# Performance work log

Hardware: AMD Instinct MI355X
Metric: run time of the kernel (lower is better)

## Reference

```python
import jax, jax.numpy as jnp
import numpy as np

INF = 1000000.0
B, S, D = 4, 1024, 768
NH, DH = 12, 64
LN_EPS = 1e-9


def _relative_shift_gather(pos_attn, context_len, shift):
    # pos_attn: [b, n, seq_len, max_rel_len]
    b, n, s, m = pos_attn.shape
    x = pos_attn.reshape(b, n, m, s)[:, :, shift:, :]
    x = x.reshape(b, n, s, m - shift)[..., :context_len]
    return x


def setup_inputs() -> dict:
    key = jax.random.key(0)
    ks = jax.random.split(key, 24)
    std = 0.02
    inp = {
        'query': jax.random.normal(ks[0], (B, S, D), jnp.float32),
        'key': jax.random.normal(ks[1], (B, S, D), jnp.float32),
        'value': jax.random.normal(ks[2], (B, S, D), jnp.float32),
        'r': jax.random.normal(ks[3], (2 * S - 1, D), jnp.float32),
        'token_type_mat': jax.random.randint(ks[4], (B, S, S), 0, 2) > 0,
        'attention_mask': jnp.ones((B, S), jnp.int32),
        'cls_mask': jnp.ones((1, 1, S, S), jnp.float32),
        'Wq': jax.random.normal(ks[5], (D, NH * DH), jnp.float32) * std,
        'Wk': jax.random.normal(ks[6], (D, NH * DH), jnp.float32) * std,
        'bk': jnp.zeros((NH * DH,), jnp.float32),
        'Wv': jax.random.normal(ks[7], (D, NH * DH), jnp.float32) * std,
        'bv': jnp.zeros((NH * DH,), jnp.float32),
        'Wpost': jax.random.normal(ks[8], (NH * DH, D), jnp.float32) * std,
        'bpost': jnp.zeros((D,), jnp.float32),
        'ln_g': jnp.ones((D,), jnp.float32),
        'ln_b': jnp.zeros((D,), jnp.float32),
        'r_w_bias': jax.random.normal(ks[9], (NH, DH), jnp.float32) * std,
        'r_r_bias': jax.random.normal(ks[10], (NH, DH), jnp.float32) * std,
        'r_kernel': jax.random.normal(ks[11], (D, NH, DH), jnp.float32) * std,
        'r_s_bias': jax.random.normal(ks[12], (NH, DH), jnp.float32) * std,
        'seg_embed': jax.random.normal(ks[13], (2, NH, DH), jnp.float32) * std,
    }
    return inp


def reference(query, key, value, r, token_type_mat, attention_mask, cls_mask,
              Wq, Wk, bk, Wv, bv, Wpost, bpost, ln_g, ln_b,
              r_w_bias, r_r_bias, r_kernel, r_s_bias, seg_embed):
    b, s, d_model = query.shape
    n_head, d_head = r_w_bias.shape
    context_len = key.shape[1]
    scale = 1.0 / d_head ** 0.5

    q_head = (query @ Wq).reshape(b, s, n_head, d_head) * scale   # bind
    k_head = (key @ Wk + bk).reshape(b, context_len, n_head, d_head)
    v_head = (value @ Wv + bv).reshape(b, context_len, n_head, d_head)

    # content score
    content_score = jnp.einsum('bind,bjnd->bnij', q_head + r_w_bias * scale, k_head)

    # relative positional attention (relative_shift path, shift=1 since s == context_len)
    shift = 2 if s != context_len else 1
    r_head = jnp.einsum('td,dnh->tnh', r, r_kernel)
    positional_attn = jnp.einsum('binh,tnh->bnit', q_head + r_r_bias * scale, r_head)
    positional_attn = _relative_shift_gather(positional_attn, context_len, shift)
    positional_attn = positional_attn * cls_mask

    # relative token-type (segment) attention
    token_type_bias = jnp.einsum('bind,snd->bnis', q_head + r_s_bias * scale, seg_embed)
    diff_tt = token_type_bias[..., 0:1]  # [b,n,i,1]
    same_tt = token_type_bias[..., 1:2]
    token_type_attn = jnp.where(token_type_mat[:, None], same_tt, diff_tt) * cls_mask

    attn_score = content_score + positional_attn + token_type_attn
    attn_score = attn_score - INF * (1.0 - attention_mask[:, None, None].astype(jnp.float32))
    attn_prob = jax.nn.softmax(attn_score, axis=-1)

    attn_vec = jnp.einsum('bnij,bjnd->bind', attn_prob, v_head)
    attn_out = attn_vec.reshape(b, s, n_head * d_head) @ Wpost + bpost

    x = query + attn_out
    mean = jnp.mean(x, axis=-1, keepdims=True)
    var = jnp.var(x, axis=-1, keepdims=True)
    out = (x - mean) * jax.lax.rsqrt(var + LN_EPS) * ln_g + ln_b
    return out
```

## Files before the change

kernel.cpp:

```cpp
#include <hip/hip_runtime.h>
#include <hip/hip_bf16.h>

#define S_LEN   1024
#define D_MODEL 768
#define N_HEAD  12
#define D_HEAD  64
#define BATCH   4
#define T_LEN   2047
#define INF_VAL 1000000.0f
#define SCALE   0.125f
#define LN_EPSF 1e-9f

typedef __attribute__((ext_vector_type(8))) __bf16 bf8;
typedef __attribute__((ext_vector_type(4))) __bf16 bf4;
typedef __attribute__((ext_vector_type(4))) float  f32x4;

__device__ __forceinline__ int swz_addr(int row, int byte_in_row) {
    return ((row << 7) + byte_in_row) ^ ((row & 7) << 4);
}

#define GLOAD_LDS(gsrc, ldst) \
    __builtin_amdgcn_global_load_lds( \
        (const __attribute__((address_space(1))) void*)(gsrc), \
        (__attribute__((address_space(3))) void*)(ldst), 16, 0, 0)

__global__ void detect_kernel(const unsigned char* __restrict__ p, int* __restrict__ flag)
{
    int lane = threadIdx.x;
    int nz = 0;
    int base = lane * 64;
    for (int k = base; k < base + 64; k += 4)
        nz += (p[k+1] != 0) + (p[k+2] != 0) + (p[k+3] != 0);
    unsigned long long m = __ballot(nz != 0);
    if (lane == 0) { flag[0] = (m == 0ull) ? 1 : 0; flag[1] = 1; }
}

__global__ __launch_bounds__(256)
void tobf16_kernel(const float* __restrict__ q, const float* __restrict__ k,
                   const float* __restrict__ v, const float* __restrict__ r,
                   __bf16* __restrict__ qb, __bf16* __restrict__ kb,
                   __bf16* __restrict__ vb, __bf16* __restrict__ rb)
{
    int z = blockIdx.z;
    const float* src; __bf16* dst; size_t n;
    if (z == 0)      { src = q; dst = qb; n = (size_t)4096*768; }
    else if (z == 1) { src = k; dst = kb; n = (size_t)4096*768; }
    else if (z == 2) { src = v; dst = vb; n = (size_t)4096*768; }
    else             { src = r; dst = rb; n = (size_t)T_LEN*768; }
    size_t i = ((size_t)blockIdx.x * 256 + threadIdx.x) * 8;
    if (i + 8 > n) return;
    float4 a = *(const float4*)(src + i);
    float4 b = *(const float4*)(src + i + 4);
    bf8 o;
    o[0]=(__bf16)a.x; o[1]=(__bf16)a.y; o[2]=(__bf16)a.z; o[3]=(__bf16)a.w;
    o[4]=(__bf16)b.x; o[5]=(__bf16)b.y; o[6]=(__bf16)b.z; o[7]=(__bf16)b.w;
    *(bf8*)(dst + i) = o;
}

__global__ __launch_bounds__(256)
void prep_sel(const void* __restrict__ ttm, const int* __restrict__ flag,
              unsigned char* __restrict__ selbit)
{
    size_t idx = ((size_t)blockIdx.x * 256 + threadIdx.x) * 8;
    unsigned long long out = 0;
    if (flag[0]) {
        const int* ip = (const int*)ttm + idx;
        int4 a = *(const int4*)ip;
        int4 b = *(const int4*)(ip + 4);
        out  = (a.x ? 1ull : 0)       | (a.y ? 1ull : 0) << 8
             | (a.z ? 1ull : 0) << 16 | (a.w ? 1ull : 0) << 24
             | (b.x ? 1ull : 0) << 32 | (b.y ? 1ull : 0) << 40
             | (b.z ? 1ull : 0) << 48 | (b.w ? 1ull : 0) << 56;
    } else {
        unsigned long long raw = *(const unsigned long long*)((const unsigned char*)ttm + idx);
        #pragma unroll
        for (int i = 0; i < 8; ++i)
            out |= (((raw >> (8*i)) & 0xffull) ? 1ull : 0) << (8*i);
    }
    *(unsigned long long*)(selbit + idx) = out;
}

__global__ __launch_bounds__(256)
void clsb_prep(const float* __restrict__ cls, const int* __restrict__ amask,
               __bf16* __restrict__ clsb, float* __restrict__ maskadd,
               int* __restrict__ flag)
{
    size_t idx = ((size_t)blockIdx.x * 256 + threadIdx.x) * 8;
    const float* p = cls + idx;
    float4 a = *(const float4*)p;
    float4 b = *(const float4*)(p + 4);
    bf8 o;
    o[0]=(__bf16)a.x; o[1]=(__bf16)a.y; o[2]=(__bf16)a.z; o[3]=(__bf16)a.w;
    o[4]=(__bf16)b.x; o[5]=(__bf16)b.y; o[6]=(__bf16)b.z; o[7]=(__bf16)b.w;
    *(bf8*)(clsb + idx) = o;
    int ok = (a.x==1.f)&&(a.y==1.f)&&(a.z==1.f)&&(a.w==1.f)
          && (b.x==1.f)&&(b.y==1.f)&&(b.z==1.f)&&(b.w==1.f);
    if (blockIdx.x == 0) {
        for (int j = threadIdx.x; j < BATCH * S_LEN; j += 256) {
            int am = amask[j];
            maskadd[j] = -INF_VAL * (1.f - (float)am);
            ok &= (am == 1);
        }
    }
    ok = __syncthreads_and(ok);
    if (threadIdx.x == 0 && !ok) atomicAnd(flag + 1, 0);
}

__global__ __launch_bounds__(256)
void wtrans_kernel(const float* __restrict__ W0, const float* __restrict__ W1,
                   const float* __restrict__ W2, const float* __restrict__ W3,
                   const float* __restrict__ W4,
                   __bf16* __restrict__ T0, __bf16* __restrict__ T1,
                   __bf16* __restrict__ T2, __bf16* __restrict__ T3,
                   __bf16* __restrict__ T4)
{
    const float* W; __bf16* Wt;
    switch (blockIdx.z) {
        case 0: W = W0; Wt = T0; break;
        case 1: W = W1; Wt = T1; break;
        case 2: W = W2; Wt = T2; break;
        case 3: W = W3; Wt = T3; break;
        default: W = W4; Wt = T4; break;
    }
    const int K = 768, N = 768;
    __shared__ float tile[64][65];
    int tid = threadIdx.x;
    int r = tid >> 4, c4 = (tid & 15) * 4;
    int k0 = blockIdx.y * 64, n0 = blockIdx.x * 64;
    #pragma unroll
    for (int rep = 0; rep < 4; ++rep) {
        int row = rep * 16 + r;
        float4 v = *(const float4*)(W + (size_t)(k0 + row) * N + n0 + c4);
        tile[row][c4+0] = v.x; tile[row][c4+1] = v.y;
        tile[row][c4+2] = v.z; tile[row][c4+3] = v.w;
    }
    __syncthreads();
    #pragma unroll
    for (int rep = 0; rep < 4; ++rep) {
        int row = rep * 16 + r;
        bf4 o;
        #pragma unroll
        for (int j = 0; j < 4; ++j) o[j] = (__bf16)tile[c4 + j][row];
        *(bf4*)(Wt + (size_t)(n0 + row) * K + k0 + c4) = o;
    }
}

__device__ __forceinline__
void gemm_tile_body(const __bf16* __restrict__ A, const __bf16* __restrict__ Bt,
                    const float* __restrict__ bias, void* __restrict__ C,
                    int M, int N, int K, float scale, int has_bias,
                    int out_mode, int m0, int n0, __bf16* As, __bf16* Bs)
{
    int tid = threadIdx.x;
    int lane = tid & 63, w = tid >> 6;
    int grp = lane >> 4, lcol = lane & 15;
    int wm = w >> 1, wn = w & 1;

    auto loadA = [&](int kt, int rep) -> bf8 {
        int id = rep * 256 + tid;
        int row = id >> 3, ch = id & 7;
        int gm = m0 + row; if (gm >= M) gm = M - 1;
        return *(const bf8*)(A + (size_t)gm * K + kt + ch * 8);
    };
    auto loadB = [&](int kt, int rep) -> bf8 {
        int id = rep * 256 + tid;
        int row = id >> 3, ch = id & 7;
        return *(const bf8*)(Bt + (size_t)(n0 + row) * K + kt + ch * 8);
    };

    bf8 aR0 = loadA(0,0), aR1 = loadA(0,1), aR2 = loadA(0,2), aR3 = loadA(0,3);
    bf8 bR0 = loadB(0,0), bR1 = loadB(0,1), bR2 = loadB(0,2), bR3 = loadB(0,3);

    f32x4 acc[4][4] = {};

    for (int kt = 0; kt < K; kt += 64) {
        __syncthreads();
        {
            int id0 = tid;
            { int id = 0*256 + id0; int row = id >> 3, ch = id & 7;
              *(bf8*)((char*)As + swz_addr(row, ch*16)) = aR0;
              *(bf8*)((char*)Bs + swz_addr(row, ch*16)) = bR0; }
            { int id = 1*256 + id0; int row = id >> 3, ch = id & 7;
              *(bf8*)((char*)As + swz_addr(row, ch*16)) = aR1;
              *(bf8*)((char*)Bs + swz_addr(row, ch*16)) = bR1; }
            { int id = 2*256 + id0; int row = id >> 3, ch = id & 7;
              *(bf8*)((char*)As + swz_addr(row, ch*16)) = aR2;
              *(bf8*)((char*)Bs + swz_addr(row, ch*16)) = bR2; }
            { int id = 3*256 + id0; int row = id >> 3, ch = id & 7;
              *(bf8*)((char*)As + swz_addr(row, ch*16)) = aR3;
              *(bf8*)((char*)Bs + swz_addr(row, ch*16)) = bR3; }
        }
        __syncthreads();
        if (kt + 64 < K) {
            aR0 = loadA(kt+64,0); aR1 = loadA(kt+64,1); aR2 = loadA(kt+64,2); aR3 = loadA(kt+64,3);
            bR0 = loadB(kt+64,0); bR1 = loadB(kt+64,1); bR2 = loadB(kt+64,2); bR3 = loadB(kt+64,3);
        }
        #pragma unroll
        for (int kk = 0; kk < 2; ++kk) {
            bf8 a[4], bb[4];
            #pragma unroll
            for (int mi = 0; mi < 4; ++mi)
                a[mi] = *(const bf8*)((const char*)As + swz_addr(wm * 64 + mi * 16 + lcol, kk * 64 + grp * 16));
            #pragma unroll
            for (int ni = 0; ni < 4; ++ni)
                bb[ni] = *(const bf8*)((const char*)Bs + swz_addr(wn * 64 + ni * 16 + lcol, kk * 64 + grp * 16));
            #pragma unroll
            for (int mi = 0; mi < 4; ++mi) {
                #pragma unroll
                for (int ni = 0; ni < 4; ++ni)
                    acc[mi][ni] = __builtin_amdgcn_mfma_f32_16x16x32_bf16(a[mi], bb[ni], acc[mi][ni], 0, 0, 0);
            }
        }
    }

    #pragma unroll
    for (int ni = 0; ni < 4; ++ni) {
        int col = n0 + wn * 64 + ni * 16 + lcol;
        float bval = has_bias ? bias[col] : 0.f;
        #pragma unroll
        for (int mi = 0; mi < 4; ++mi) {
            int rbase = m0 + wm * 64 + mi * 16 + grp * 4;
            if (out_mode == 2) {
                int hn = col >> 6, d = col & 63;
                int bb2 = rbase >> 10;
                int j = rbase & 1023;
                bf4 o;
                #pragma unroll
                for (int reg = 0; reg < 4; ++reg)
                    o[reg] = (__bf16)(acc[mi][ni][reg] * scale + bval);
                *(bf4*)((__bf16*)C + ((size_t)(bb2 * N_HEAD + hn) * 64 + d) * 1024 + j) = o;
            } else {
                #pragma unroll
                for (int reg = 0; reg < 4; ++reg) {
                    int row = rbase + reg;
                    if (row < M) {
                        float vv = acc[mi][ni][reg] * scale + bval;
                        if (out_mode == 1) ((__bf16*)C)[(size_t)row * N + col] = (__bf16)vv;
                        else               ((float*)C)[(size_t)row * N + col] = vv;
                    }
                }
            }
        }
    }
}

__global__ __launch_bounds__(256, 3)
void proj_gemm(const __bf16* __restrict__ qb, const __bf16* __restrict__ kb,
               const __bf16* __restrict__ vb, const __bf16* __restrict__ rb,
               const __bf16* __restrict__ Wqt, const __bf16* __restrict__ Wkt,
               const __bf16* __restrict__ Wvt, const __bf16* __restrict__ rkt,
               const float* __restrict__ bk, const float* __restrict__ bv,
               __bf16* __restrict__ qh, __bf16* __restrict__ kh,
               __bf16* __restrict__ vhT, __bf16* __restrict__ rhd)
{
    __shared__ __align__(16) __bf16 As[128 * 64];
    __shared__ __align__(16) __bf16 Bs[128 * 64];
    int id = blockIdx.x;
    int wg = (id & 7) * 96 + (id >> 3);
    int z  = wg / 192;
    int rem = wg % 192;
    int by = rem / 6, bx = rem % 6;

    const __bf16* A; const __bf16* Bt; const float* bias; void* C;
    int M; float scale; int has_bias; int omode;
    if (z == 0)      { A = qb; Bt = Wqt; bias = nullptr; C = qh;  M = 4096; scale = SCALE; has_bias = 0; omode = 1; }
    else if (z == 1) { A = kb; Bt = Wkt; bias = bk;      C = kh;  M = 4096; scale = 1.f;   has_bias = 1; omode = 1; }
    else if (z == 2) { A = vb; Bt = Wvt; bias = bv;      C = vhT; M = 4096; scale = 1.f;   has_bias = 1; omode = 2; }
    else             { A = rb; Bt = rkt; bias = nullptr; C = rhd; M = T_LEN; scale = 1.f;  has_bias = 0; omode = 1; }
    int m0 = by * 128, n0 = bx * 128;
    if (m0 >= M) return;
    gemm_tile_body(A, Bt, bias, C, M, 768, 768, scale, has_bias, omode, m0, n0, As, Bs);
}

__global__ __launch_bounds__(256, 3)
void post_gemm(const __bf16* __restrict__ av, const __bf16* __restrict__ Wpt,
               const float* __restrict__ bpost, float* __restrict__ ao)
{
    __shared__ __align__(16) __bf16 As[128 * 64];
    __shared__ __align__(16) __bf16 Bs[128 * 64];
    int id = blockIdx.x;
    int wg = (id & 7) * 24 + (id >> 3);
    int by = wg / 6, bx = wg % 6;
    gemm_tile_body(av, Wpt, bpost, ao, 4096, 768, 768, 1.f, 1, 0,
                   by * 128, bx * 128, As, Bs);
}

__global__ __launch_bounds__(256)
void ttbias_kernel(const __bf16* __restrict__ qh, const float* __restrict__ rsb,
                   const float* __restrict__ seg, float* __restrict__ tt)
{
    int idx = blockIdx.x * 256 + threadIdx.x;
    if (idx >= BATCH * S_LEN * N_HEAD * 2) return;
    int s2  = idx & 1;
    int n   = (idx >> 1) % N_HEAD;
    int row = idx / (2 * N_HEAD);
    const __bf16* q  = qh  + (size_t)row * D_MODEL + n * D_HEAD;
    const float* sg = seg + ((size_t)s2 * N_HEAD + n) * D_HEAD;
    const float* rb = rsb + n * D_HEAD;
    float s = 0.f;
    for (int h = 0; h < D_HEAD; ++h) s += ((float)q[h] + rb[h] * SCALE) * sg[h];
    tt[idx] = s;
}

__global__ __launch_bounds__(256, 3)
void attn_kernel(const __bf16* __restrict__ qh, const __bf16* __restrict__ kh,
                 const __bf16* __restrict__ vhT, const __bf16* __restrict__ rhd,
                 const float* __restrict__ tt, const __bf16* __restrict__ clsb,
                 const unsigned char* __restrict__ selbit,
                 const float* __restrict__ maskadd,
                 const float* __restrict__ rwb, const float* __restrict__ rrb,
                 const int* __restrict__ flag, __bf16* __restrict__ av)
{
    __shared__ __align__(16) __bf16 Kt[64*64];
    __shared__ __align__(16) __bf16 Vt[64*64];
    __shared__ __align__(16) __bf16 Rw[128*64];
    __shared__ __align__(16) __bf16 Ps[4*16*64];
    __shared__ __align__(16) __bf16 poss[4*16*84];

    int tid = threadIdx.x;
    int i0 = blockIdx.x * 64;
    int n  = blockIdx.y;
    int b  = blockIdx.z;
    int bS = b * S_LEN;
    int n64 = n * D_HEAD;
    int simple = flag[1];

    int lane = tid & 63, w = tid >> 6;
    int grp = lane >> 4, lcol = lane & 15;

    const __bf16* vT = vhT + (size_t)(b * N_HEAD + n) * 64 * 1024;

    int srow = tid >> 3;
    int koff = (((tid & 7) * 16) ^ ((srow & 7) << 4)) >> 1;

    bf8 qwA[2], qrA[2];
    {
        size_t qrow = (size_t)(bS + i0 + w*16 + lcol) * D_MODEL + n64;
        #pragma unroll
        for (int kk = 0; kk < 2; ++kk) {
            int kb = kk*32 + grp*8;
            bf8 qv = *(const bf8*)(qh + qrow + kb);
            const float* wbp = rwb + n64 + kb;
            const float* rbp = rrb + n64 + kb;
            #pragma unroll
            for (int q = 0; q < 8; ++q) {
                float f = (float)qv[q];
                qwA[kk][q] = (__bf16)(f + wbp[q] * SCALE);
                qrA[kk][q] = (__bf16)(f + rbp[q] * SCALE);
            }
        }
    }

    float t0r[4], t1r[4];
    #pragma unroll
    for (int reg = 0; reg < 4; ++reg) {
        int gi = i0 + w*16 + grp*4 + reg;
        const float* ttrow = tt + (((size_t)(bS + gi)) * N_HEAD + n) * 2;
        t0r[reg] = ttrow[0];
        t1r[reg] = ttrow[1];
    }

    float fixv = 0.f;
    if (i0 == 0) {
        float qv = (float)qh[((size_t)(bS + 1)) * D_MODEL + n64 + lane] + rrb[n64 + lane] * SCALE;
        float rv = (float)rhd[n64 + lane];
        float t = qv * rv;
        #pragma unroll
        for (int m = 32; m; m >>= 1) t += __shfl_xor(t, m, 64);
        fixv = t;
    }
    bool fix = (i0 == 0 && w == 0 && lane == 15);

    float m_run[4] = {-1e30f, -1e30f, -1e30f, -1e30f};
    float l_run[4] = {0.f, 0.f, 0.f, 0.f};
    f32x4 acc[4] = {};
    const f32x4 zero4 = {0.f, 0.f, 0.f, 0.f};

    for (int jt = 0; jt < 16; ++jt) {
        int j0 = jt * 64;
        int w0 = j0 - i0 + 961;
        __syncthreads();

        {
            const __bf16* ks = kh + (size_t)(bS + j0 + srow) * D_MODEL + n64 + koff;
            GLOAD_LDS(ks,                      (char*)Kt + w*1024);
            GLOAD_LDS(ks + (size_t)32*D_MODEL, (char*)Kt + 4096 + w*1024);
        }
        {
            const __bf16* vs = vT + (size_t)srow * 1024 + j0 + koff;
            GLOAD_LDS(vs,             (char*)Vt + w*1024);
            GLOAD_LDS(vs + 32*1024,   (char*)Vt + 4096 + w*1024);
        }
        if (jt == 0) {
            #pragma unroll
            for (int rep = 0; rep < 4; ++rep) {
                int idx = rep*256 + tid;
                int rowl = idx >> 3;
                int c8  = (idx & 7) * 8;
                int t = w0 + rowl;
                bf8 v = {};
                if (t < T_LEN)
                    v = *(const bf8*)(rhd + (size_t)t * D_MODEL + n64 + c8);
                *(bf8*)((char*)Rw + swz_addr(t & 127, c8*2)) = v;
            }
        } else {
            #pragma unroll
            for (int rep = 0; rep < 2; ++rep) {
                int idx = rep*256 + tid;
                int rowl = idx >> 3;
                int c8  = (idx & 7) * 8;
                int t = w0 + 64 + rowl;
                bf8 v = {};
                if (t < T_LEN)
                    v = *(const bf8*)(rhd + (size_t)t * D_MODEL + n64 + c8);
                *(bf8*)((char*)Rw + swz_addr(t & 127, c8*2)) = v;
            }
        }
        __syncthreads();

        f32x4 sc_[4] = {zero4, zero4, zero4, zero4};
        #pragma unroll
        for (int c = 0; c < 4; ++c) {
            #pragma unroll
            for (int kk = 0; kk < 2; ++kk) {
                bf8 kb2 = *(const bf8*)((const char*)Kt + swz_addr(c*16 + lcol, kk*64 + grp*16));
                sc_[c] = __builtin_amdgcn_mfma_f32_16x16x32_bf16(qwA[kk], kb2, sc_[c], 0, 0, 0);
            }
        }
        int a0 = 3 - w;
        f32x4 pacc[5] = {zero4, zero4, zero4, zero4, zero4};
        #pragma unroll
        for (int pa = 0; pa < 5; ++pa) {
            #pragma unroll
            for (int kk = 0; kk < 2; ++kk) {
                int tr = w0 + (a0 + pa) * 16 + lcol;
                bf8 rb2 = *(const bf8*)((const char*)Rw + swz_addr(tr & 127, kk*64 + grp*16));
                pacc[pa] = __builtin_amdgcn_mfma_f32_16x16x32_bf16(qrA[kk], rb2, pacc[pa], 0, 0, 0);
            }
        }
        __bf16* pw = poss + w * 16 * 84;
        #pragma unroll
        for (int pa = 0; pa < 5; ++pa) {
            #pragma unroll
            for (int reg = 0; reg < 4; ++reg)
                pw[(grp*4 + reg) * 84 + pa*16 + lcol] = (__bf16)pacc[pa][reg];
        }
        asm volatile("s_waitcnt lgkmcnt(0)" ::: "memory");
        __builtin_amdgcn_sched_barrier(0);

        float sv[4][4];
        if (simple) {
            #pragma unroll
            for (int c = 0; c < 4; ++c) {
                int jl = c*16 + lcol;
                int gj = j0 + jl;
                #pragma unroll
                for (int reg = 0; reg < 4; ++reg) {
                    int il = grp*4 + reg;
                    int gi = i0 + w*16 + il;
                    int rr = jl - il + 15;
                    float pv = (float)pw[il * 84 + rr];
                    if (fix && jt == 15 && c == 3 && reg == 0) pv = fixv;
                    float ttv = selbit[((size_t)(bS + gi)) * S_LEN + gj] ? t1r[reg] : t0r[reg];
                    sv[c][reg] = sc_[c][reg] + pv + ttv;
                }
            }
        } else {
            #pragma unroll
            for (int c = 0; c < 4; ++c) {
                int jl = c*16 + lcol;
                int gj = j0 + jl;
                float ma = maskadd[b * S_LEN + gj];
                #pragma unroll
                for (int reg = 0; reg < 4; ++reg) {
                    int il = grp*4 + reg;
                    int gi = i0 + w*16 + il;
                    int rr = jl - il + 15;
                    float pv = (float)pw[il * 84 + rr];
                    if (fix && jt == 15 && c == 3 && reg == 0) pv = fixv;
                    float clv = (float)clsb[(size_t)gi * S_LEN + gj];
                    float ttv = selbit[((size_t)(bS + gi)) * S_LEN + gj] ? t1r[reg] : t0r[reg];
                    sv[c][reg] = sc_[c][reg] + clv * (pv + ttv) + ma;
                }
            }
        }

        float mx[4], alpha[4], rs[4];
        #pragma unroll
        for (int reg = 0; reg < 4; ++reg)
            mx[reg] = fmaxf(fmaxf(sv[0][reg], sv[1][reg]), fmaxf(sv[2][reg], sv[3][reg]));
        #pragma unroll
        for (int msk = 1; msk < 16; msk <<= 1) {
            #pragma unroll
            for (int reg = 0; reg < 4; ++reg)
                mx[reg] = fmaxf(mx[reg], __shfl_xor(mx[reg], msk, 64));
        }
        #pragma unroll
        for (int reg = 0; reg < 4; ++reg) {
            float mn = fmaxf(m_run[reg], mx[reg]);
            alpha[reg] = __expf(m_run[reg] - mn);
            m_run[reg] = mn;
            rs[reg] = 0.f;
        }
        __bf16* psw = Ps;
        #pragma unroll
        for (int c = 0; c < 4; ++c) {
            int jl = c*16 + lcol;
            #pragma unroll
            for (int reg = 0; reg < 4; ++reg) {
                int il = grp*4 + reg;
                float p = __expf(sv[c][reg] - m_run[reg]);
                rs[reg] += p;
                *((__bf16*)((char*)psw + w*2048 + swz_addr(il, jl*2))) = (__bf16)p;
            }
        }
        #pragma unroll
        for (int msk = 1; msk < 16; msk <<= 1) {
            #pragma unroll
            for (int reg = 0; reg < 4; ++reg)
                rs[reg] += __shfl_xor(rs[reg], msk, 64);
        }
        #pragma unroll
        for (int reg = 0; reg < 4; ++reg)
            l_run[reg] = l_run[reg] * alpha[reg] + rs[reg];
        #pragma unroll
        for (int c = 0; c < 4; ++c) {
            #pragma unroll
            for (int reg = 0; reg < 4; ++reg) acc[c][reg] *= alpha[reg];
        }
        asm volatile("s_waitcnt lgkmcnt(0)" ::: "memory");
        __builtin_amdgcn_sched_barrier(0);

        bf8 pA[2];
        #pragma unroll
        for (int kk = 0; kk < 2; ++kk)
            pA[kk] = *(const bf8*)((const char*)psw + w*2048 + swz_addr(lcol, kk*64 + grp*16));
        #pragma unroll
        for (int c = 0; c < 4; ++c) {
            #pragma unroll
            for (int kk = 0; kk < 2; ++kk) {
                bf8 vb2 = *(const bf8*)((const char*)Vt + swz_addr(c*16 + lcol, kk*64 + grp*16));
                acc[c] = __builtin_amdgcn_mfma_f32_16x16x32_bf16(pA[kk], vb2, acc[c], 0, 0, 0);
            }
        }
    }

    float inv[4];
    #pragma unroll
    for (int reg = 0; reg < 4; ++reg) inv[reg] = 1.f / l_run[reg];
    #pragma unroll
    for (int c = 0; c < 4; ++c) {
        #pragma unroll
        for (int reg = 0; reg < 4; ++reg) {
            size_t o = ((size_t)(bS + i0 + w*16 + grp*4 + reg)) * D_MODEL + n64 + c*16 + lcol;
            av[o] = (__bf16)(acc[c][reg] * inv[reg]);
        }
    }
}

__global__ __launch_bounds__(256)
void ln_kernel(const float* __restrict__ query, const float* __restrict__ ao,
               const float* __restrict__ gam, const float* __restrict__ bet,
               float* __restrict__ out)
{
    int row = blockIdx.x;
    int tid = threadIdx.x;
    size_t base = (size_t)row * D_MODEL;
    float xv[3];
    float s = 0.f, sq = 0.f;
    #pragma unroll
    for (int k = 0; k < 3; ++k) {
        int c = tid + k * 256;
        float v = query[base + c] + ao[base + c];
        xv[k] = v; s += v; sq += v * v;
    }
    for (int off = 32; off > 0; off >>= 1) {
        s  += __shfl_down(s, off);
        sq += __shfl_down(sq, off);
    }
    __shared__ float rs[4], rq[4];
    __shared__ float mean_s, inv_s;
    int wid = tid >> 6, lane = tid & 63;
    if (lane == 0) { rs[wid] = s; rq[wid] = sq; }
    __syncthreads();
    if (tid == 0) {
        float S0 = rs[0] + rs[1] + rs[2] + rs[3];
        float Q0 = rq[0] + rq[1] + rq[2] + rq[3];
        float mean = S0 / (float)D_MODEL;
        float var  = Q0 / (float)D_MODEL - mean * mean;
        mean_s = mean;
        inv_s  = rsqrtf(var + LN_EPSF);
    }
    __syncthreads();
    float mean = mean_s, inv = inv_s;
    #pragma unroll
    for (int k = 0; k < 3; ++k) {
        int c = tid + k * 256;
        out[base + c] = (xv[k] - mean) * inv * gam[c] + bet[c];
    }
}

extern "C" void kernel_launch(void* const* d_in, const int* in_sizes, int n_in,
                              void* d_out, int out_size, void* d_ws, size_t ws_size,
                              hipStream_t stream)
{
    const float* query = (const float*)d_in[0];
    const float* key   = (const float*)d_in[1];
    const float* value = (const float*)d_in[2];
    const float* r     = (const float*)d_in[3];
    const void*  ttm   = d_in[4];
    const int*   amask = (const int*)d_in[5];
    const float* cls   = (const float*)d_in[6];
    const float* Wq    = (const float*)d_in[7];
    const float* Wk    = (const float*)d_in[8];
    const float* bk    = (const float*)d_in[9];
    const float* Wv    = (const float*)d_in[10];
    const float* bv    = (const float*)d_in[11];
    const float* Wpost = (const float*)d_in[12];
    const float* bpost = (const float*)d_in[13];
    const float* ln_g  = (const float*)d_in[14];
    const float* ln_b  = (const float*)d_in[15];
    const float* rwb   = (const float*)d_in[16];
    const float* rrb   = (const float*)d_in[17];
    const float* rker  = (const float*)d_in[18];
    const float* rsb   = (const float*)d_in[19];
    const float* seg   = (const float*)d_in[20];

    char* wsb = (char*)d_ws;
    __bf16* qh  = (__bf16*)(wsb);
    __bf16* kh  = (__bf16*)(wsb + 6291456);
    __bf16* vhT = (__bf16*)(wsb + 12582912);
    __bf16* rhd = (__bf16*)(wsb + 18874368);
    float*  tt  = (float*) (wsb + 22020096);
    __bf16* av  = (__bf16*)(wsb + 22413312);
    float*  ao  = (float*) (wsb + 28704768);
    __bf16* Wqt = (__bf16*)(wsb + 41287680);
    __bf16* Wkt = (__bf16*)(wsb + 42467328);
    __bf16* Wvt = (__bf16*)(wsb + 43646976);
    __bf16* Wpt = (__bf16*)(wsb + 44826624);
    __bf16* rkt = (__bf16*)(wsb + 46006272);
    int*    flag = (int*)  (wsb + 47185920);
    unsigned char* selbit = (unsigned char*)(wsb + 47186176);
    __bf16* clsb    = (__bf16*)(wsb + 51380480);
    float*  maskadd = (float*) (wsb + 53477632);
    __bf16* rin_b   = (__bf16*)(wsb + 53494016);

    __bf16* qin_b = av;
    __bf16* kin_b = (__bf16*)ao;
    __bf16* vin_b = (__bf16*)(wsb + 34996224);

    detect_kernel<<<1, 64, 0, stream>>>((const unsigned char*)ttm, flag);
    tobf16_kernel<<<dim3(1536, 1, 4), 256, 0, stream>>>(query, key, value, r,
                                                        qin_b, kin_b, vin_b, rin_b);
    prep_sel<<<2048, 256, 0, stream>>>(ttm, flag, selbit);
    clsb_prep<<<512, 256, 0, stream>>>(cls, amask, clsb, maskadd, flag);

    dim3 gtr(12, 12, 5);
    wtrans_kernel<<<gtr, 256, 0, stream>>>(Wq, Wk, Wv, Wpost, rker,
                                           Wqt, Wkt, Wvt, Wpt, rkt);

    proj_gemm<<<768, 256, 0, stream>>>(qin_b, kin_b, vin_b, rin_b,
                                       Wqt, Wkt, Wvt, rkt, bk, bv,
                                       qh, kh, vhT, rhd);

    ttbias_kernel<<<384, 256, 0, stream>>>(qh, rsb, seg, tt);

    dim3 gattn(16, 12, 4);
    attn_kernel<<<gattn, 256, 0, stream>>>(qh, kh, vhT, rhd, tt, clsb, selbit,
                                           maskadd, rwb, rrb, flag, av);

    post_gemm<<<192, 256, 0, stream>>>(av, Wpt, bpost, ao);

    ln_kernel<<<4096, 256, 0, stream>>>(query, ao, ln_g, ln_b, (float*)d_out);
}
```

Before: 170.0 us.

## Bit-pack token-type selector and register-prefetch relative-position rows in attention

The token-type selector changes from one byte per (i,j) pair to one bit per pair, packed into 64-bit words. The attention kernel loads one word per row per key tile, which replaces a scattered byte load for every score element. Separately, the relative-position R rows for the next tile are prefetched into registers after the barrier, and the LDS store at the start of the next iteration uses those registers, so the global-load latency overlaps with compute. The cost is extra registers per thread, which could reduce occupancy under the existing launch bounds of 256 threads and 3 blocks.

Measured after the change: 250.2 us. 1.47x slower.

```diff
diff --git a/kernel.cpp b/kernel.cpp
--- a/kernel.cpp
+++ b/kernel.cpp
@@ -59,25 +59,31 @@
 
 __global__ __launch_bounds__(256)
 void prep_sel(const void* __restrict__ ttm, const int* __restrict__ flag,
-              unsigned char* __restrict__ selbit)
-{
-    size_t idx = ((size_t)blockIdx.x * 256 + threadIdx.x) * 8;
+              unsigned long long* __restrict__ selpack)
+{
+    size_t widx = (size_t)blockIdx.x * 256 + threadIdx.x;
     unsigned long long out = 0;
     if (flag[0]) {
-        const int* ip = (const int*)ttm + idx;
-        int4 a = *(const int4*)ip;
-        int4 b = *(const int4*)(ip + 4);
-        out  = (a.x ? 1ull : 0)       | (a.y ? 1ull : 0) << 8
-             | (a.z ? 1ull : 0) << 16 | (a.w ? 1ull : 0) << 24
-             | (b.x ? 1ull : 0) << 32 | (b.y ? 1ull : 0) << 40
-             | (b.z ? 1ull : 0) << 48 | (b.w ? 1ull : 0) << 56;
+        const int* ip = (const int*)ttm + widx * 64;
+        #pragma unroll
+        for (int g = 0; g < 16; ++g) {
+            int4 a = *(const int4*)(ip + g * 4);
+            unsigned long long nib = (a.x ? 1u : 0u) | (a.y ? 2u : 0u)
+                                   | (a.z ? 4u : 0u) | (a.w ? 8u : 0u);
+            out |= nib << (g * 4);
+        }
     } else {
-        unsigned long long raw = *(const unsigned long long*)((const unsigned char*)ttm + idx);
-        #pragma unroll
-        for (int i = 0; i < 8; ++i)
-            out |= (((raw >> (8*i)) & 0xffull) ? 1ull : 0) << (8*i);
-    }
-    *(unsigned long long*)(selbit + idx) = out;
+        const unsigned long long* p8 =
+            (const unsigned long long*)((const unsigned char*)ttm + widx * 64);
+        #pragma unroll
+        for (int g = 0; g < 8; ++g) {
+            unsigned long long raw = p8[g];
+            #pragma unroll
+            for (int k = 0; k < 8; ++k)
+                if ((raw >> (8*k)) & 0xffull) out |= 1ull << (g*8 + k);
+        }
+    }
+    selpack[widx] = out;
 }
 
 __global__ __launch_bounds__(256)
@@ -306,7 +312,7 @@
 void attn_kernel(const __bf16* __restrict__ qh, const __bf16* __restrict__ kh,
                  const __bf16* __restrict__ vhT, const __bf16* __restrict__ rhd,
                  const float* __restrict__ tt, const __bf16* __restrict__ clsb,
-                 const unsigned char* __restrict__ selbit,
+                 const unsigned long long* __restrict__ selpack,
                  const float* __restrict__ maskadd,
                  const float* __restrict__ rwb, const float* __restrict__ rrb,
                  const int* __restrict__ flag, __bf16* __restrict__ av)
@@ -332,6 +338,7 @@
 
     int srow = tid >> 3;
     int koff = (((tid & 7) * 16) ^ ((srow & 7) << 4)) >> 1;
+    int c8s  = (tid & 7) * 8;
 
     bf8 qwA[2], qrA[2];
     {
@@ -376,9 +383,30 @@
     f32x4 acc[4] = {};
     const f32x4 zero4 = {0.f, 0.f, 0.f, 0.f};
 
+    int w0_0 = -i0 + 961;
+
+    bf8 rRa, rRb, rRc, rRd;
+    {
+        int rowl = tid >> 3;
+        int t0 = w0_0 + rowl;
+        rRa = (t0      >= 0 && t0      < T_LEN) ? *(const bf8*)(rhd + (size_t)(t0     ) * D_MODEL + n64 + c8s) : bf8{};
+        rRb = (t0+32   >= 0 && t0+32   < T_LEN) ? *(const bf8*)(rhd + (size_t)(t0+32  ) * D_MODEL + n64 + c8s) : bf8{};
+        rRc = (t0+64   >= 0 && t0+64   < T_LEN) ? *(const bf8*)(rhd + (size_t)(t0+64  ) * D_MODEL + n64 + c8s) : bf8{};
+        rRd = (t0+96   >= 0 && t0+96   < T_LEN) ? *(const bf8*)(rhd + (size_t)(t0+96  ) * D_MODEL + n64 + c8s) : bf8{};
+    }
+
     for (int jt = 0; jt < 16; ++jt) {
         int j0 = jt * 64;
         int w0 = j0 - i0 + 961;
+        int rowl = tid >> 3;
+
+        unsigned long long selw[4];
+        #pragma unroll
+        for (int reg = 0; reg < 4; ++reg) {
+            int gi = i0 + w*16 + grp*4 + reg;
+            selw[reg] = selpack[(size_t)(bS + gi) * 16 + jt];
+        }
+
         __syncthreads();
 
         {
@@ -392,31 +420,23 @@
             GLOAD_LDS(vs + 32*1024,   (char*)Vt + 4096 + w*1024);
         }
         if (jt == 0) {
-            #pragma unroll
-            for (int rep = 0; rep < 4; ++rep) {
-                int idx = rep*256 + tid;
-                int rowl = idx >> 3;
-                int c8  = (idx & 7) * 8;
-                int t = w0 + rowl;
-                bf8 v = {};
-                if (t < T_LEN)
-                    v = *(const bf8*)(rhd + (size_t)t * D_MODEL + n64 + c8);
-                *(bf8*)((char*)Rw + swz_addr(t & 127, c8*2)) = v;
-            }
+            int t0 = w0 + rowl;
+            *(bf8*)((char*)Rw + swz_addr( t0       & 127, c8s*2)) = rRa;
+            *(bf8*)((char*)Rw + swz_addr((t0 + 32) & 127, c8s*2)) = rRb;
+            *(bf8*)((char*)Rw + swz_addr((t0 + 64) & 127, c8s*2)) = rRc;
+            *(bf8*)((char*)Rw + swz_addr((t0 + 96) & 127, c8s*2)) = rRd;
         } else {
-            #pragma unroll
-            for (int rep = 0; rep < 2; ++rep) {
-                int idx = rep*256 + tid;
-                int rowl = idx >> 3;
-                int c8  = (idx & 7) * 8;
-                int t = w0 + 64 + rowl;
-                bf8 v = {};
-                if (t < T_LEN)
-                    v = *(const bf8*)(rhd + (size_t)t * D_MODEL + n64 + c8);
-                *(bf8*)((char*)Rw + swz_addr(t & 127, c8*2)) = v;
-            }
+            int t0 = w0 + 64 + rowl;
+            *(bf8*)((char*)Rw + swz_addr( t0       & 127, c8s*2)) = rRa;
+            *(bf8*)((char*)Rw + swz_addr((t0 + 32) & 127, c8s*2)) = rRb;
         }
         __syncthreads();
+
+        if (jt < 15) {
+            int tN = w0 + 128 + rowl;
+            rRa = (tN      < T_LEN) ? *(const bf8*)(rhd + (size_t)(tN     ) * D_MODEL + n64 + c8s) : bf8{};
+            rRb = (tN + 32 < T_LEN) ? *(const bf8*)(rhd + (size_t)(tN + 32) * D_MODEL + n64 + c8s) : bf8{};
+        }
 
         f32x4 sc_[4] = {zero4, zero4, zero4, zero4};
         #pragma unroll
@@ -453,15 +473,13 @@
             #pragma unroll
             for (int c = 0; c < 4; ++c) {
                 int jl = c*16 + lcol;
-                int gj = j0 + jl;
                 #pragma unroll
                 for (int reg = 0; reg < 4; ++reg) {
                     int il = grp*4 + reg;
-                    int gi = i0 + w*16 + il;
                     int rr = jl - il + 15;
                     float pv = (float)pw[il * 84 + rr];
                     if (fix && jt == 15 && c == 3 && reg == 0) pv = fixv;
-                    float ttv = selbit[((size_t)(bS + gi)) * S_LEN + gj] ? t1r[reg] : t0r[reg];
+                    float ttv = ((selw[reg] >> jl) & 1ull) ? t1r[reg] : t0r[reg];
                     sv[c][reg] = sc_[c][reg] + pv + ttv;
                 }
             }
@@ -479,7 +497,7 @@
                     float pv = (float)pw[il * 84 + rr];
                     if (fix && jt == 15 && c == 3 && reg == 0) pv = fixv;
                     float clv = (float)clsb[(size_t)gi * S_LEN + gj];
-                    float ttv = selbit[((size_t)(bS + gi)) * S_LEN + gj] ? t1r[reg] : t0r[reg];
+                    float ttv = ((selw[reg] >> jl) & 1ull) ? t1r[reg] : t0r[reg];
                     sv[c][reg] = sc_[c][reg] + clv * (pv + ttv) + ma;
                 }
             }
@@ -640,7 +658,7 @@
     __bf16* Wpt = (__bf16*)(wsb + 44826624);
     __bf16* rkt = (__bf16*)(wsb + 46006272);
     int*    flag = (int*)  (wsb + 47185920);
-    unsigned char* selbit = (unsigned char*)(wsb + 47186176);
+    unsigned long long* selpack = (unsigned long long*)(wsb + 47186176);
     __bf16* clsb    = (__bf16*)(wsb + 51380480);
     float*  maskadd = (float*) (wsb + 53477632);
     __bf16* rin_b   = (__bf16*)(wsb + 53494016);
@@ -652,7 +670,7 @@
     detect_kernel<<<1, 64, 0, stream>>>((const unsigned char*)ttm, flag);
     tobf16_kernel<<<dim3(1536, 1, 4), 256, 0, stream>>>(query, key, value, r,
                                                         qin_b, kin_b, vin_b, rin_b);
-    prep_sel<<<2048, 256, 0, stream>>>(ttm, flag, selbit);
+    prep_sel<<<256, 256, 0, stream>>>(ttm, flag, selpack);
     clsb_prep<<<512, 256, 0, stream>>>(cls, amask, clsb, maskadd, flag);
 
     dim3 gtr(12, 12, 5);
@@ -666,7 +684,7 @@
     ttbias_kernel<<<384, 256, 0, stream>>>(qh, rsb, seg, tt);
 
     dim3 gattn(16, 12, 4);
-    attn_kernel<<<gattn, 256, 0, stream>>>(qh, kh, vhT, rhd, tt, clsb, selbit,
+    attn_kernel<<<gattn, 256, 0, stream>>>(qh, kh, vhT, rhd, tt, clsb, selpack,
                                            maskadd, rwb, rrb, flag, av);
 
     post_gemm<<<192, 256, 0, stream>>>(av, Wpt, bpost, ao);
```
